# Kernel optimization log

Hardware: AMD Instinct MI355X
Metric: run time of the kernel (lower is better)

## Reference

```python
import jax, jax.numpy as jnp
import numpy as np

# Dimensions (see init_kwargs): C=out_channels, R=res, PS=pool_size, HN=head_num,
# D=head_dim=R*R//HN, input spatial H=W=PS*R.
B, C, R, PS, HN, D = 16, 512, 32, 3, 8, 128
NORM_C = 0.5


def _avg_pool(x, k):
    b, c, h, w = x.shape
    return x.reshape(b, c, h // k, k, w // k, k).mean(axis=(3, 5))


def _max_pool(x, k):
    b, c, h, w = x.shape
    return x.reshape(b, c, h // k, k, w // k, k).max(axis=(3, 5))


def _to_heads(p):
    # Replicates torch: [B,C,R,R].view(B,R*R,C).permute(0,2,1).view(B,C,HN,D).permute(0,2,1,3)
    t = p.reshape(B, R * R, C).transpose(0, 2, 1)  # [B, C, R*R]
    return t.reshape(B, C, HN, D).transpose(0, 2, 1, 3)  # [B, HN, C, D]


def setup_inputs() -> dict:
    key = jax.random.key(0)
    ks = jax.random.split(key, 6)
    H = PS * R
    x = jax.random.normal(ks[0], (B, C, H, H), jnp.float32)
    # per-head q/k projections (Linear(head_dim, head_dim) per head)
    Wqk = jax.random.normal(ks[1], (HN, D, D), jnp.float32) * (1.0 / np.sqrt(D))
    bqk = jax.random.normal(ks[2], (HN, D), jnp.float32) * 0.01
    # w_p: Linear(C, C) feeding sigmoid gate
    Wp = jax.random.normal(ks[3], (C, C), jnp.float32) * (1.0 / np.sqrt(C))
    bp = jnp.zeros((C,), jnp.float32)
    # w_v: 1x1 Conv2d(C, C)
    Wv = jax.random.normal(ks[4], (C, C), jnp.float32) * (1.0 / np.sqrt(C))
    bv = jax.random.normal(ks[5], (C,), jnp.float32) * 0.01
    return {"x": x, "Wqk": Wqk, "bqk": bqk, "Wp": Wp, "bp": bp,
            "Wv": Wv, "bv": bv, "weight": 0}


def reference(x, Wqk, bqk, Wp, bp, Wv, bv, weight):
    # pooled query / key token grids: [B, C, R, R]
    q_pool = _avg_pool(x, PS)
    k_pool = _max_pool(x, PS)

    # heads over channels: [B, HN, C, D], then per-head linear (torch Linear: y = x W^T + b)
    q = jnp.einsum('bhcd,hed->bhce', _to_heads(q_pool), Wqk) + bqk[None, :, None, :]
    k = jnp.einsum('bhcd,hed->bhce', _to_heads(k_pool), Wqk) + bqk[None, :, None, :]

    # value: 1x1 conv then AvgPool2d(3) -> [B, HN, C, D]
    v_conv = jnp.einsum('bchw,oc->bohw', x, Wv) + bv[None, :, None, None]
    v = _to_heads(_avg_pool(v_conv, 3))

    # channel attention scores: [B, HN, C, C]
    scores = jnp.einsum('bhcd,bhed->bhce', q, k)
    # learned power-law exponent gate: sigmoid(Linear(mean over keys))
    p = jax.nn.sigmoid(scores.mean(axis=-1) @ Wp.T + bp)  # [B, HN, C]
    norm_scores = scores / jnp.power(jnp.float32(D), NORM_C + p[..., None])
    w = jax.nn.softmax(norm_scores, axis=-1)
    attn = jnp.einsum('bhce,bhed->bhcd', w, v)  # [B, HN, C, D]

    # back to [B, R, R, C] (torch permute/view chain)
    attn = attn.transpose(0, 2, 1, 3).reshape(B, C, R * R)
    attn = attn.transpose(0, 2, 1).reshape(B, R, R, C)

    # residual on pooled input (original code's residual shape is inconsistent;
    # we use the pooled token grid, same reshape path as the output)
    resid = q_pool.reshape(B, R * R, C).reshape(B, R, R, C)
    return resid + attn * (1 + weight)
```

## Files before the change

### kernel.cpp

```cpp
#include <hip/hip_runtime.h>
#include <math.h>

typedef unsigned short u16;
typedef short bf16x8 __attribute__((ext_vector_type(8)));
typedef float floatx4 __attribute__((ext_vector_type(4)));

#define F_QP   0ull
#define F_IPW  8388608ull
#define F_WPT  8454144ull
#define F_END  8716288ull
#define U_QPT_V 0ull
#define U_QPT_P 8388608ull
#define U_KPT_P 16777216ull
#define U_PQ    25165824ull
#define U_PK    33554432ull
#define U_VP    41943040ull
#define U_WV    50331648ull
#define U_WQK   50593792ull

__device__ __forceinline__ u16 f2bf(float f) {
    union { float f; unsigned u; } v; v.f = f;
    return (u16)((v.u + 0x7fffu + ((v.u >> 16) & 1u)) >> 16);
}
__device__ __forceinline__ float bf2f(u16 u) {
    union { unsigned u; float f; } v; v.u = ((unsigned)u) << 16;
    return v.f;
}
__device__ __forceinline__ void ld_async16(const u16* g, u16* l) {
    __builtin_amdgcn_global_load_lds(
        (const __attribute__((address_space(1))) void*)g,
        (__attribute__((address_space(3))) void*)l, 16, 0, 0);
}

__global__ __launch_bounds__(256) void pool_fused(const float* __restrict__ x,
                                                  float* __restrict__ qp,
                                                  u16* __restrict__ qpT_v,
                                                  u16* __restrict__ qpT_p,
                                                  u16* __restrict__ kpT_p) {
    __shared__ float Tq[32][33], Tk[32][33];
    const int tid = threadIdx.x;
    const int i  = blockIdx.x;
    const int c0 = blockIdx.y * 32;
    const int b  = blockIdx.z;
    const int j  = tid & 31, cg = tid >> 5;
    #pragma unroll
    for (int p = 0; p < 4; ++p) {
        int cl = p * 8 + cg;
        const float* px = x + (size_t)b * 4718592 + (size_t)(c0 + cl) * 9216 + (3 * i) * 96 + 3 * j;
        float s = 0.f, mx = -INFINITY;
        #pragma unroll
        for (int di = 0; di < 3; ++di)
            #pragma unroll
            for (int dj = 0; dj < 3; ++dj) {
                float v = px[di * 96 + dj];
                s += v; mx = fmaxf(mx, v);
            }
        float q = s * (1.f / 9.f);
        Tq[cl][j] = q; Tk[cl][j] = mx;
        qp[(size_t)b * 524288 + (size_t)(c0 + cl) * 1024 + i * 32 + j] = q;
    }
    __syncthreads();
    const int cl = tid & 31, jq = tid >> 5;
    const int rh = i >> 4;
    const int s2 = (c0 + cl) * 2 + rh;
    #pragma unroll
    for (int jj = 0; jj < 4; ++jj) {
        int jw = jq + jj * 8;
        int rr = i * 32 + jw;
        int cc = rr & 511;
        u16 qb = f2bf(Tq[cl][jw]);
        u16 kb = f2bf(Tk[cl][jw]);
        qpT_v[(size_t)b * 524288 + (size_t)rr * 512 + c0 + cl] = qb;
        qpT_p[(size_t)b * 524288 + (size_t)cc * 1024 + s2] = qb;
        kpT_p[(size_t)b * 524288 + (size_t)cc * 1024 + s2] = kb;
    }
}

__global__ __launch_bounds__(256) void cvt_w(const float* __restrict__ Wv,
                                             const float* __restrict__ Wqk,
                                             u16* __restrict__ Wv_bf,
                                             u16* __restrict__ Wqk_bf) {
    int i = blockIdx.x * 256 + threadIdx.x;
    if (i < 262144) Wv_bf[i] = f2bf(Wv[i]);
    else if (i < 393216) Wqk_bf[i - 262144] = f2bf(Wqk[i - 262144]);
}

__global__ __launch_bounds__(256) void transpose_wp(const float* __restrict__ in,
                                                    float* __restrict__ out) {
    __shared__ float t[32][33];
    int x0 = blockIdx.x * 32, y0 = blockIdx.y * 32;
    int tx = threadIdx.x & 31, ty = threadIdx.x >> 5;
    #pragma unroll
    for (int it = 0; it < 4; ++it)
        t[ty + it * 8][tx] = in[(size_t)(y0 + ty + it * 8) * 512 + x0 + tx];
    __syncthreads();
    #pragma unroll
    for (int it = 0; it < 4; ++it)
        out[(size_t)(x0 + ty + it * 8) * 512 + y0 + tx] = t[tx][ty + it * 8];
}

__device__ __forceinline__ void gemm_bt_body(const u16* __restrict__ A, int ldA,
                                             const u16* __restrict__ B, int ldB, int K,
                                             u16* As, u16* Bs, floatx4 (&acc)[4][4]) {
    const int tid = threadIdx.x;
    const int lane = tid & 63;
    const int wv = tid >> 6;
    const int wm = (wv & 1) * 64, wn = (wv >> 1) * 64;
    const u16* ga0 = A + (size_t)(tid >> 2) * ldA + (tid & 3) * 8;
    const u16* ga1 = A + (size_t)((tid >> 2) + 64) * ldA + (tid & 3) * 8;
    const u16* gb0 = B + (size_t)(tid >> 2) * ldB + (tid & 3) * 8;
    const u16* gb1 = B + (size_t)((tid >> 2) + 64) * ldB + (tid & 3) * 8;
    u16* la0 = As + tid * 8;
    u16* la1 = As + (tid + 256) * 8;
    u16* lb0 = Bs + tid * 8;
    u16* lb1 = Bs + (tid + 256) * 8;
    const int arow = (lane & 15) * 32 + (lane >> 4) * 8;
    for (int k0 = 0; k0 < K; k0 += 32) {
        ld_async16(ga0 + k0, la0);
        ld_async16(ga1 + k0, la1);
        ld_async16(gb0 + k0, lb0);
        ld_async16(gb1 + k0, lb1);
        __syncthreads();
        bf16x8 af[4], bfr[4];
        #pragma unroll
        for (int i = 0; i < 4; ++i)
            af[i] = *(const bf16x8*)&As[(wm + i * 16) * 32 + arow];
        #pragma unroll
        for (int j = 0; j < 4; ++j)
            bfr[j] = *(const bf16x8*)&Bs[(wn + j * 16) * 32 + arow];
        #pragma unroll
        for (int i = 0; i < 4; ++i)
            #pragma unroll
            for (int j = 0; j < 4; ++j)
                acc[i][j] = __builtin_amdgcn_mfma_f32_16x16x32_bf16(af[i], bfr[j], acc[i][j], 0, 0, 0);
        __syncthreads();
    }
}

__global__ __launch_bounds__(256) void vpool_mfma(const u16* __restrict__ Wv_bf,
                                                  const float* __restrict__ bv,
                                                  const u16* __restrict__ qpT_v,
                                                  u16* __restrict__ vp_bf) {
    __shared__ __align__(16) u16 As[4096], Bs[4096];
    floatx4 acc[4][4] = {};
    const int m0 = blockIdx.y * 128, n0 = blockIdx.x * 128, b = blockIdx.z;
    gemm_bt_body(Wv_bf + (size_t)m0 * 512, 512,
                 qpT_v + (size_t)b * 524288 + (size_t)n0 * 512, 512, 512, As, Bs, acc);
    const int tid = threadIdx.x, lane = tid & 63, wv = tid >> 6;
    const int wm = (wv & 1) * 64, wn = (wv >> 1) * 64, col = lane & 15, quad = lane >> 4;
    u16* outb = vp_bf + (size_t)b * 524288;
    #pragma unroll
    for (int i = 0; i < 4; ++i)
        #pragma unroll
        for (int r = 0; r < 4; ++r) {
            int m = m0 + wm + i * 16 + quad * 4 + r;
            float bias = bv[m];
            #pragma unroll
            for (int j = 0; j < 4; ++j) {
                int n = n0 + wn + j * 16 + col;
                outb[(size_t)m * 1024 + n] = f2bf(acc[i][j][r] + bias);
            }
        }
}

__global__ __launch_bounds__(256) void proj_mfma(const u16* __restrict__ qpT_p,
                                                 const u16* __restrict__ kpT_p,
                                                 const u16* __restrict__ Wqk_bf,
                                                 const float* __restrict__ bqk,
                                                 u16* __restrict__ pq_bf,
                                                 u16* __restrict__ pk_bf) {
    __shared__ __align__(16) u16 As[4096], Bs[4096];
    floatx4 acc[4][4] = {};
    const int z = blockIdx.y;
    const int b = z >> 4, h = (z >> 1) & 7, src = z & 1;
    const int m0 = blockIdx.x * 128;
    const u16* P = (src ? kpT_p : qpT_p) + (size_t)b * 524288 + (size_t)m0 * 1024 + h * 128;
    gemm_bt_body(P, 1024, Wqk_bf + h * 16384, 128, 128, As, Bs, acc);
    const int tid = threadIdx.x, lane = tid & 63, wv = tid >> 6;
    const int wm = (wv & 1) * 64, wn = (wv >> 1) * 64, col = lane & 15, quad = lane >> 4;
    u16* outp = (src ? pk_bf : pq_bf) + (size_t)(b * 8 + h) * 65536 + (size_t)m0 * 128;
    #pragma unroll
    for (int i = 0; i < 4; ++i)
        #pragma unroll
        for (int r = 0; r < 4; ++r) {
            int m = wm + i * 16 + quad * 4 + r;
            #pragma unroll
            for (int j = 0; j < 4; ++j) {
                int n = wn + j * 16 + col;
                outp[(size_t)m * 128 + n] = f2bf(acc[i][j][r] + bqk[h * 128 + n]);
            }
        }
}

__global__ __launch_bounds__(256) void gate_fused(const u16* __restrict__ pq_bf,
                                                  const u16* __restrict__ pk_bf,
                                                  const float* __restrict__ WpT,
                                                  const float* __restrict__ bp,
                                                  float* __restrict__ ipw) {
    __shared__ float sp[256];
    __shared__ float kb[128];
    __shared__ float ms[512];
    const int bh = blockIdx.x, tid = threadIdx.x;
    const u16* pkb = pk_bf + (size_t)bh * 65536;
    const u16* pqb = pq_bf + (size_t)bh * 65536;
    {
        int d = tid & 127, half = tid >> 7;
        const u16* p = pkb + (size_t)(half * 256) * 128 + d;
        float s = 0.f;
        #pragma unroll 8
        for (int e = 0; e < 256; ++e) s += bf2f(p[(size_t)e * 128]);
        sp[tid] = s;
    }
    __syncthreads();
    if (tid < 128) kb[tid] = (sp[tid] + sp[tid + 128]) * (1.f / 512.f);
    __syncthreads();
    for (int cc = tid; cc < 512; cc += 256) {
        const u16* q = pqb + (size_t)cc * 128;
        float s = 0.f;
        #pragma unroll 8
        for (int d = 0; d < 128; ++d) s += bf2f(q[d]) * kb[d];
        ms[cc] = s;
    }
    __syncthreads();
    for (int c2 = tid; c2 < 512; c2 += 256) {
        float a = bp[c2];
        #pragma unroll 4
        for (int c = 0; c < 512; ++c) a += ms[c] * WpT[(size_t)c * 512 + c2];
        float pg = 1.f / (1.f + __expf(-a));
        ipw[bh * 512 + c2] = exp2f(-7.f * (0.5f + pg));
    }
}

__global__ __launch_bounds__(256, 2) void flash_mfma(const u16* __restrict__ pq_bf,
                                                     const u16* __restrict__ pk_bf,
                                                     const u16* __restrict__ vp_bf,
                                                     const float* __restrict__ ipw,
                                                     const float* __restrict__ qp,
                                                     float* __restrict__ outp,
                                                     const int* __restrict__ wgt) {
    __shared__ __align__(16) u16 As[4096];
    __shared__ __align__(16) u16 Bs[4096];
    __shared__ __align__(16) u16 Et[128 * 136];
    __shared__ float rsS[128];
    __shared__ float ipwS[128];
    const int tid = threadIdx.x, lane = tid & 63, wv = tid >> 6;
    const int wm = (wv & 1) * 64, wn = (wv >> 1) * 64, col = lane & 15, quad = lane >> 4;
    const int bh = blockIdx.y, b = bh >> 3, h = bh & 7;
    const int m0 = blockIdx.x * 128;
    if (tid < 128) { rsS[tid] = 0.f; ipwS[tid] = ipw[bh * 512 + m0 + tid]; }
    const u16* Aq = pq_bf + (size_t)bh * 65536 + (size_t)m0 * 128;
    const u16* Bk = pk_bf + (size_t)bh * 65536;
    const u16* Av = vp_bf + (size_t)b * 524288 + (size_t)h * 65536;
    const int srow = tid >> 2, scol = (tid & 3) * 8;
    u16 *la0 = As + tid * 8, *la1 = As + (tid + 256) * 8;
    u16 *lb0 = Bs + tid * 8, *lb1 = Bs + (tid + 256) * 8;
    const int arow = col * 32 + quad * 8;
    floatx4 accP[4][4] = {};
    __syncthreads();

    for (int n0 = 0; n0 < 512; n0 += 128) {
        floatx4 accS[4][4] = {};
        for (int k0 = 0; k0 < 128; k0 += 32) {
            ld_async16(Aq + (size_t)srow * 128 + k0 + scol, la0);
            ld_async16(Aq + (size_t)(srow + 64) * 128 + k0 + scol, la1);
            ld_async16(Bk + (size_t)(n0 + srow) * 128 + k0 + scol, lb0);
            ld_async16(Bk + (size_t)(n0 + srow + 64) * 128 + k0 + scol, lb1);
            __syncthreads();
            bf16x8 af[4], bfr[4];
            #pragma unroll
            for (int i = 0; i < 4; ++i) af[i] = *(const bf16x8*)&As[(wm + i * 16) * 32 + arow];
            #pragma unroll
            for (int j = 0; j < 4; ++j) bfr[j] = *(const bf16x8*)&Bs[(wn + j * 16) * 32 + arow];
            #pragma unroll
            for (int i = 0; i < 4; ++i)
                #pragma unroll
                for (int j = 0; j < 4; ++j)
                    accS[i][j] = __builtin_amdgcn_mfma_f32_16x16x32_bf16(af[i], bfr[j], accS[i][j], 0, 0, 0);
            __syncthreads();
        }
        #pragma unroll
        for (int i = 0; i < 4; ++i)
            #pragma unroll
            for (int r = 0; r < 4; ++r) {
                int ml = wm + i * 16 + quad * 4 + r;
                float sc = ipwS[ml];
                float p = 0.f;
                #pragma unroll
                for (int j = 0; j < 4; ++j) {
                    float e = __expf(accS[i][j][r] * sc);
                    p += e;
                    Et[ml * 136 + wn + j * 16 + col] = f2bf(e);
                }
                #pragma unroll
                for (int o = 8; o; o >>= 1) p += __shfl_xor(p, o);
                if (col == 0) atomicAdd(&rsS[ml], p);
            }
        __syncthreads();
        for (int k0 = 0; k0 < 128; k0 += 32) {
            ld_async16(Av + (size_t)srow * 512 + n0 + k0 + scol, la0);
            ld_async16(Av + (size_t)(srow + 64) * 512 + n0 + k0 + scol, la1);
            __syncthreads();
            bf16x8 af[4], bfr[4];
            #pragma unroll
            for (int i = 0; i < 4; ++i) af[i] = *(const bf16x8*)&As[(wm + i * 16) * 32 + arow];
            #pragma unroll
            for (int j = 0; j < 4; ++j) bfr[j] = *(const bf16x8*)&Et[(wn + j * 16 + col) * 136 + k0 + quad * 8];
            #pragma unroll
            for (int i = 0; i < 4; ++i)
                #pragma unroll
                for (int j = 0; j < 4; ++j)
                    accP[i][j] = __builtin_amdgcn_mfma_f32_16x16x32_bf16(af[i], bfr[j], accP[i][j], 0, 0, 0);
            __syncthreads();
        }
    }
    const float mult = 1.f + (float)wgt[0];
    #pragma unroll
    for (int j = 0; j < 4; ++j) {
        int nl = wn + j * 16 + col;
        float inv = mult / rsS[nl];
        #pragma unroll
        for (int i = 0; i < 4; ++i)
            #pragma unroll
            for (int r = 0; r < 4; ++r) {
                int d = wm + i * 16 + quad * 4 + r;
                size_t o = (size_t)b * 524288 + (size_t)(h * 128 + d) * 512 + m0 + nl;
                outp[o] = qp[o] + accP[i][j][r] * inv;
            }
    }
}

extern "C" void kernel_launch(void* const* d_in, const int* in_sizes, int n_in,
                              void* d_out, int out_size, void* d_ws, size_t ws_size,
                              hipStream_t stream) {
    const float* x   = (const float*)d_in[0];
    const float* Wqk = (const float*)d_in[1];
    const float* bqk = (const float*)d_in[2];
    const float* Wp  = (const float*)d_in[3];
    const float* bp  = (const float*)d_in[4];
    const float* Wv  = (const float*)d_in[5];
    const float* bv  = (const float*)d_in[6];
    const int*   wgt = (const int*)d_in[7];
    float* out = (float*)d_out;

    float* ws = (float*)d_ws;
    float* qp  = ws + F_QP;
    float* ipw = ws + F_IPW;
    float* WpT = ws + F_WPT;
    u16* ub = (u16*)(ws + F_END);
    u16* qpT_v  = ub + U_QPT_V;
    u16* qpT_p  = ub + U_QPT_P;
    u16* kpT_p  = ub + U_KPT_P;
    u16* pq_bf  = ub + U_PQ;
    u16* pk_bf  = ub + U_PK;
    u16* vp_bf  = ub + U_VP;
    u16* Wv_bf  = ub + U_WV;
    u16* Wqk_bf = ub + U_WQK;

    pool_fused<<<dim3(32, 16, 16), 256, 0, stream>>>(x, qp, qpT_v, qpT_p, kpT_p);
    cvt_w<<<1536, 256, 0, stream>>>(Wv, Wqk, Wv_bf, Wqk_bf);
    transpose_wp<<<dim3(16, 16), 256, 0, stream>>>(Wp, WpT);
    vpool_mfma<<<dim3(8, 4, 16), 256, 0, stream>>>(Wv_bf, bv, qpT_v, vp_bf);
    proj_mfma<<<dim3(4, 256), 256, 0, stream>>>(qpT_p, kpT_p, Wqk_bf, bqk, pq_bf, pk_bf);
    gate_fused<<<128, 256, 0, stream>>>(pq_bf, pk_bf, WpT, bp, ipw);
    flash_mfma<<<dim3(4, 128), 256, 0, stream>>>(pq_bf, pk_bf, vp_bf, ipw, qp, out, wgt);
}
```

Baseline: 598.3 us.

## Stage pool input in LDS, merge weight-prep and GEMM kernels, vectorize gate loads

```diff
diff --git a/kernel.cpp b/kernel.cpp
--- a/kernel.cpp
+++ b/kernel.cpp
@@ -4,6 +4,7 @@
 typedef unsigned short u16;
 typedef short bf16x8 __attribute__((ext_vector_type(8)));
 typedef float floatx4 __attribute__((ext_vector_type(4)));
+typedef unsigned short ushort4v __attribute__((ext_vector_type(4)));
 
 #define F_QP   0ull
 #define F_IPW  8388608ull
@@ -37,16 +38,29 @@
                                                   u16* __restrict__ qpT_v,
                                                   u16* __restrict__ qpT_p,
                                                   u16* __restrict__ kpT_p) {
+    __shared__ __align__(16) float Xs[9216];
     __shared__ float Tq[32][33], Tk[32][33];
     const int tid = threadIdx.x;
     const int i  = blockIdx.x;
     const int c0 = blockIdx.y * 32;
     const int b  = blockIdx.z;
-    const int j  = tid & 31, cg = tid >> 5;
+    {
+        const float* xb = x + (size_t)b * 4718592 + (size_t)c0 * 9216 + (3 * i) * 96;
+        float4* Xs4 = (float4*)Xs;
+        #pragma unroll
+        for (int it = 0; it < 9; ++it) {
+            int f = tid + it * 256;
+            int cl = f / 72;
+            int rem = f - cl * 72;
+            Xs4[f] = *(const float4*)(xb + (size_t)cl * 9216 + rem * 4);
+        }
+    }
+    __syncthreads();
+    const int j = tid & 31, cg = tid >> 5;
     #pragma unroll
     for (int p = 0; p < 4; ++p) {
         int cl = p * 8 + cg;
-        const float* px = x + (size_t)b * 4718592 + (size_t)(c0 + cl) * 9216 + (3 * i) * 96 + 3 * j;
+        const float* px = Xs + cl * 288 + 3 * j;
         float s = 0.f, mx = -INFINITY;
         #pragma unroll
         for (int di = 0; di < 3; ++di)
@@ -76,27 +90,34 @@
     }
 }
 
-__global__ __launch_bounds__(256) void cvt_w(const float* __restrict__ Wv,
-                                             const float* __restrict__ Wqk,
-                                             u16* __restrict__ Wv_bf,
-                                             u16* __restrict__ Wqk_bf) {
-    int i = blockIdx.x * 256 + threadIdx.x;
-    if (i < 262144) Wv_bf[i] = f2bf(Wv[i]);
-    else if (i < 393216) Wqk_bf[i - 262144] = f2bf(Wqk[i - 262144]);
-}
-
-__global__ __launch_bounds__(256) void transpose_wp(const float* __restrict__ in,
-                                                    float* __restrict__ out) {
+__global__ __launch_bounds__(256) void prep_w(const float* __restrict__ Wv,
+                                              const float* __restrict__ Wqk,
+                                              const float* __restrict__ Wp,
+                                              u16* __restrict__ Wv_bf,
+                                              u16* __restrict__ Wqk_bf,
+                                              float* __restrict__ WpT) {
     __shared__ float t[32][33];
-    int x0 = blockIdx.x * 32, y0 = blockIdx.y * 32;
-    int tx = threadIdx.x & 31, ty = threadIdx.x >> 5;
-    #pragma unroll
-    for (int it = 0; it < 4; ++it)
-        t[ty + it * 8][tx] = in[(size_t)(y0 + ty + it * 8) * 512 + x0 + tx];
-    __syncthreads();
-    #pragma unroll
-    for (int it = 0; it < 4; ++it)
-        out[(size_t)(x0 + ty + it * 8) * 512 + y0 + tx] = t[tx][ty + it * 8];
+    const int blk = blockIdx.x, tid = threadIdx.x;
+    if (blk < 384) {
+        int i = (blk * 256 + tid) * 4;
+        const float* src; u16* dst; int off;
+        if (i < 262144) { src = Wv; dst = Wv_bf; off = i; }
+        else            { src = Wqk; dst = Wqk_bf; off = i - 262144; }
+        float4 v = *(const float4*)(src + off);
+        ushort4v o; o.x = f2bf(v.x); o.y = f2bf(v.y); o.z = f2bf(v.z); o.w = f2bf(v.w);
+        *(ushort4v*)(dst + off) = o;
+    } else {
+        int bb = blk - 384;
+        int x0 = (bb & 15) * 32, y0 = (bb >> 4) * 32;
+        int tx = tid & 31, ty = tid >> 5;
+        #pragma unroll
+        for (int it = 0; it < 4; ++it)
+            t[ty + it * 8][tx] = Wp[(size_t)(y0 + ty + it * 8) * 512 + x0 + tx];
+        __syncthreads();
+        #pragma unroll
+        for (int it = 0; it < 4; ++it)
+            WpT[(size_t)(x0 + ty + it * 8) * 512 + y0 + tx] = t[tx][ty + it * 8];
+    }
 }
 
 __device__ __forceinline__ void gemm_bt_body(const u16* __restrict__ A, int ldA,
@@ -137,59 +158,58 @@
     }
 }
 
-__global__ __launch_bounds__(256) void vpool_mfma(const u16* __restrict__ Wv_bf,
+__global__ __launch_bounds__(256) void gemms_mfma(const u16* __restrict__ Wv_bf,
                                                   const float* __restrict__ bv,
                                                   const u16* __restrict__ qpT_v,
-                                                  u16* __restrict__ vp_bf) {
+                                                  u16* __restrict__ vp_bf,
+                                                  const u16* __restrict__ qpT_p,
+                                                  const u16* __restrict__ kpT_p,
+                                                  const u16* __restrict__ Wqk_bf,
+                                                  const float* __restrict__ bqk,
+                                                  u16* __restrict__ pq_bf,
+                                                  u16* __restrict__ pk_bf) {
     __shared__ __align__(16) u16 As[4096], Bs[4096];
     floatx4 acc[4][4] = {};
-    const int m0 = blockIdx.y * 128, n0 = blockIdx.x * 128, b = blockIdx.z;
-    gemm_bt_body(Wv_bf + (size_t)m0 * 512, 512,
-                 qpT_v + (size_t)b * 524288 + (size_t)n0 * 512, 512, 512, As, Bs, acc);
     const int tid = threadIdx.x, lane = tid & 63, wv = tid >> 6;
     const int wm = (wv & 1) * 64, wn = (wv >> 1) * 64, col = lane & 15, quad = lane >> 4;
-    u16* outb = vp_bf + (size_t)b * 524288;
-    #pragma unroll
-    for (int i = 0; i < 4; ++i)
-        #pragma unroll
-        for (int r = 0; r < 4; ++r) {
-            int m = m0 + wm + i * 16 + quad * 4 + r;
-            float bias = bv[m];
-            #pragma unroll
-            for (int j = 0; j < 4; ++j) {
-                int n = n0 + wn + j * 16 + col;
-                outb[(size_t)m * 1024 + n] = f2bf(acc[i][j][r] + bias);
+    const int blk = blockIdx.x;
+    if (blk < 512) {
+        const int n0 = (blk & 7) * 128, m0 = ((blk >> 3) & 3) * 128, b = blk >> 5;
+        gemm_bt_body(Wv_bf + (size_t)m0 * 512, 512,
+                     qpT_v + (size_t)b * 524288 + (size_t)n0 * 512, 512, 512, As, Bs, acc);
+        u16* outb = vp_bf + (size_t)b * 524288;
+        #pragma unroll
+        for (int i = 0; i < 4; ++i)
+            #pragma unroll
+            for (int r = 0; r < 4; ++r) {
+                int m = m0 + wm + i * 16 + quad * 4 + r;
+                float bias = bv[m];
+                #pragma unroll
+                for (int j = 0; j < 4; ++j) {
+                    int n = n0 + wn + j * 16 + col;
+                    outb[(size_t)m * 1024 + n] = f2bf(acc[i][j][r] + bias);
+                }
             }
-        }
-}
-
-__global__ __launch_bounds__(256) void proj_mfma(const u16* __restrict__ qpT_p,
-                                                 const u16* __restrict__ kpT_p,
-                                                 const u16* __restrict__ Wqk_bf,
-                                                 const float* __restrict__ bqk,
-                                                 u16* __restrict__ pq_bf,
-                                                 u16* __restrict__ pk_bf) {
-    __shared__ __align__(16) u16 As[4096], Bs[4096];
-    floatx4 acc[4][4] = {};
-    const int z = blockIdx.y;
-    const int b = z >> 4, h = (z >> 1) & 7, src = z & 1;
-    const int m0 = blockIdx.x * 128;
-    const u16* P = (src ? kpT_p : qpT_p) + (size_t)b * 524288 + (size_t)m0 * 1024 + h * 128;
-    gemm_bt_body(P, 1024, Wqk_bf + h * 16384, 128, 128, As, Bs, acc);
-    const int tid = threadIdx.x, lane = tid & 63, wv = tid >> 6;
-    const int wm = (wv & 1) * 64, wn = (wv >> 1) * 64, col = lane & 15, quad = lane >> 4;
-    u16* outp = (src ? pk_bf : pq_bf) + (size_t)(b * 8 + h) * 65536 + (size_t)m0 * 128;
-    #pragma unroll
-    for (int i = 0; i < 4; ++i)
-        #pragma unroll
-        for (int r = 0; r < 4; ++r) {
-            int m = wm + i * 16 + quad * 4 + r;
-            #pragma unroll
-            for (int j = 0; j < 4; ++j) {
-                int n = wn + j * 16 + col;
-                outp[(size_t)m * 128 + n] = f2bf(acc[i][j][r] + bqk[h * 128 + n]);
+    } else {
+        const int blk2 = blk - 512;
+        const int m0 = (blk2 & 3) * 128;
+        const int z = blk2 >> 2;
+        const int b = z >> 4, h = (z >> 1) & 7, src = z & 1;
+        const u16* P = (src ? kpT_p : qpT_p) + (size_t)b * 524288 + (size_t)m0 * 1024 + h * 128;
+        gemm_bt_body(P, 1024, Wqk_bf + h * 16384, 128, 128, As, Bs, acc);
+        u16* outp = (src ? pk_bf : pq_bf) + (size_t)(b * 8 + h) * 65536 + (size_t)m0 * 128;
+        #pragma unroll
+        for (int i = 0; i < 4; ++i)
+            #pragma unroll
+            for (int r = 0; r < 4; ++r) {
+                int m = wm + i * 16 + quad * 4 + r;
+                #pragma unroll
+                for (int j = 0; j < 4; ++j) {
+                    int n = wn + j * 16 + col;
+                    outp[(size_t)m * 128 + n] = f2bf(acc[i][j][r] + bqk[h * 128 + n]);
+                }
             }
-        }
+    }
 }
 
 __global__ __launch_bounds__(256) void gate_fused(const u16* __restrict__ pq_bf,
@@ -197,37 +217,58 @@
                                                   const float* __restrict__ WpT,
                                                   const float* __restrict__ bp,
                                                   float* __restrict__ ipw) {
-    __shared__ float sp[256];
+    __shared__ float red[16][128];
     __shared__ float kb[128];
     __shared__ float ms[512];
     const int bh = blockIdx.x, tid = threadIdx.x;
     const u16* pkb = pk_bf + (size_t)bh * 65536;
     const u16* pqb = pq_bf + (size_t)bh * 65536;
     {
-        int d = tid & 127, half = tid >> 7;
-        const u16* p = pkb + (size_t)(half * 256) * 128 + d;
+        const int dc = tid & 15, rg = tid >> 4;
+        float a[8] = {};
+        const u16* p = pkb + (size_t)rg * 4096 + dc * 8;
+        #pragma unroll 8
+        for (int r = 0; r < 32; ++r) {
+            bf16x8 v = *(const bf16x8*)(p + (size_t)r * 128);
+            #pragma unroll
+            for (int k = 0; k < 8; ++k) a[k] += bf2f((u16)v[k]);
+        }
+        #pragma unroll
+        for (int k = 0; k < 8; ++k) red[rg][dc * 8 + k] = a[k];
+    }
+    __syncthreads();
+    if (tid < 128) {
         float s = 0.f;
-        #pragma unroll 8
-        for (int e = 0; e < 256; ++e) s += bf2f(p[(size_t)e * 128]);
-        sp[tid] = s;
-    }
-    __syncthreads();
-    if (tid < 128) kb[tid] = (sp[tid] + sp[tid + 128]) * (1.f / 512.f);
+        #pragma unroll
+        for (int g = 0; g < 16; ++g) s += red[g][tid];
+        kb[tid] = s * (1.f / 512.f);
+    }
     __syncthreads();
     for (int cc = tid; cc < 512; cc += 256) {
         const u16* q = pqb + (size_t)cc * 128;
         float s = 0.f;
-        #pragma unroll 8
-        for (int d = 0; d < 128; ++d) s += bf2f(q[d]) * kb[d];
+        #pragma unroll
+        for (int ch = 0; ch < 16; ++ch) {
+            bf16x8 v = *(const bf16x8*)(q + ch * 8);
+            #pragma unroll
+            for (int k = 0; k < 8; ++k) s += bf2f((u16)v[k]) * kb[ch * 8 + k];
+        }
         ms[cc] = s;
     }
     __syncthreads();
-    for (int c2 = tid; c2 < 512; c2 += 256) {
-        float a = bp[c2];
+    {
+        const int c2 = tid * 2;
+        float a0 = bp[c2], a1 = bp[c2 + 1];
         #pragma unroll 4
-        for (int c = 0; c < 512; ++c) a += ms[c] * WpT[(size_t)c * 512 + c2];
-        float pg = 1.f / (1.f + __expf(-a));
-        ipw[bh * 512 + c2] = exp2f(-7.f * (0.5f + pg));
+        for (int c = 0; c < 512; ++c) {
+            float m = ms[c];
+            float2 w = *(const float2*)&WpT[(size_t)c * 512 + c2];
+            a0 += m * w.x; a1 += m * w.y;
+        }
+        float p0 = 1.f / (1.f + __expf(-a0));
+        float p1 = 1.f / (1.f + __expf(-a1));
+        ipw[bh * 512 + c2]     = exp2f(-7.f * (0.5f + p0));
+        ipw[bh * 512 + c2 + 1] = exp2f(-7.f * (0.5f + p1));
     }
 }
 
@@ -356,11 +397,10 @@
     u16* Wv_bf  = ub + U_WV;
     u16* Wqk_bf = ub + U_WQK;
 
+    prep_w<<<640, 256, 0, stream>>>(Wv, Wqk, Wp, Wv_bf, Wqk_bf, WpT);
     pool_fused<<<dim3(32, 16, 16), 256, 0, stream>>>(x, qp, qpT_v, qpT_p, kpT_p);
-    cvt_w<<<1536, 256, 0, stream>>>(Wv, Wqk, Wv_bf, Wqk_bf);
-    transpose_wp<<<dim3(16, 16), 256, 0, stream>>>(Wp, WpT);
-    vpool_mfma<<<dim3(8, 4, 16), 256, 0, stream>>>(Wv_bf, bv, qpT_v, vp_bf);
-    proj_mfma<<<dim3(4, 256), 256, 0, stream>>>(qpT_p, kpT_p, Wqk_bf, bqk, pq_bf, pk_bf);
+    gemms_mfma<<<1536, 256, 0, stream>>>(Wv_bf, bv, qpT_v, vp_bf,
+                                         qpT_p, kpT_p, Wqk_bf, bqk, pq_bf, pk_bf);
     gate_fused<<<128, 256, 0, stream>>>(pq_bf, pk_bf, WpT, bp, ipw);
     flash_mfma<<<dim3(4, 128), 256, 0, stream>>>(pq_bf, pk_bf, vp_bf, ipw, qp, out, wgt);
 }
```

New measurement: 582.3 us. -2.7%, faster.
